# Kernel tuning notes

Hardware: AMD Instinct MI355X
Metric: run time of the kernel (lower is better)

The kernel has to match this reference:

```python
import jax, jax.numpy as jnp
import numpy as np

EMBED_DIM = 256
NUM_HEADS = 4
HEAD_DIM = EMBED_DIM // NUM_HEADS  # 64
FEAT_X = FEAT_Y = 64               # 64*64 = 4096 tokens
THETA = 10000.0


def _axial_cos_sin(dim, end_x, end_y, theta):
    # compute_axial_cis: dim//4 frequencies per spatial axis, concatenated -> [N, dim//2]
    f = 1.0 / (theta ** (np.arange(0, dim, 4)[: dim // 4].astype(np.float32) / dim))
    t = np.arange(end_x * end_y)
    tx = (t % end_x).astype(np.float32)
    ty = (t // end_x).astype(np.float32)
    ang = np.concatenate([np.outer(tx, f), np.outer(ty, f)], axis=-1)  # [N, dim//2]
    return jnp.asarray(np.cos(ang)), jnp.asarray(np.sin(ang))


def _apply_rope(x, cos, sin):
    # x: [B, H, N, D]; adjacent pairs (x[..., 2i], x[..., 2i+1]) are the complex parts
    xr = x.reshape(*x.shape[:-1], -1, 2)
    xa, xb = xr[..., 0], xr[..., 1]          # [B, H, N, D//2]
    oa = xa * cos - xb * sin                  # cos/sin: [N, D//2], broadcast
    ob = xa * sin + xb * cos
    return jnp.stack([oa, ob], axis=-1).reshape(x.shape)


def setup_inputs() -> dict:
    key = jax.random.key(0)
    ks = jax.random.split(key, 8)
    B, N, D = 1, FEAT_X * FEAT_Y, EMBED_DIM
    s = 0.02  # weight init scale
    return {
        "q": jax.random.normal(ks[0], (B, N, D), jnp.float32),
        "k": jax.random.normal(ks[1], (B, N, D), jnp.float32),
        "v": jax.random.normal(ks[2], (B, N, D), jnp.float32),
        "wq": jax.random.normal(ks[3], (D, D), jnp.float32) * s,
        "bq": jnp.zeros((D,), jnp.float32),
        "wk": jax.random.normal(ks[4], (D, D), jnp.float32) * s,
        "bk": jnp.zeros((D,), jnp.float32),
        "wv": jax.random.normal(ks[5], (D, D), jnp.float32) * s,
        "bv": jnp.zeros((D,), jnp.float32),
        "wo": jax.random.normal(ks[6], (D, D), jnp.float32) * s,
        "bo": jnp.zeros((D,), jnp.float32),
        "return_attn": 0,
        "num_k_exclude_rope": 0,
    }


def reference(q, k, v, wq, bq, wk, bk, wv, bv, wo, bo, return_attn, num_k_exclude_rope):
    B, Nq, D = q.shape
    H, hd = NUM_HEADS, HEAD_DIM
    # QKV projections (weights stored [in, out], equiv to torch Linear W.T)
    qp = (q @ wq + bq).reshape(B, Nq, H, hd).transpose(0, 2, 1, 3)   # [B,H,Nq,hd]
    kp = (k @ wk + bk).reshape(B, -1, H, hd).transpose(0, 2, 1, 3)   # [B,H,Nk,hd]
    vp = (v @ wv + bv).reshape(B, -1, H, hd).transpose(0, 2, 1, 3)
    # rotary encoding on q and the first (Nk - num_k_exclude_rope) keys
    cos, sin = _axial_cos_sin(hd, FEAT_X, FEAT_Y, THETA)
    qp = _apply_rope(qp, cos, sin)
    nkr = kp.shape[2] - num_k_exclude_rope  # static Python int
    if num_k_exclude_rope > 0:
        kp = jnp.concatenate([_apply_rope(kp[:, :, :nkr], cos, sin), kp[:, :, nkr:]], axis=2)
    else:
        kp = _apply_rope(kp, cos, sin)
    # SDPA (eval: dropout_p = 0)
    scale = 1.0 / jnp.sqrt(jnp.asarray(hd, qp.dtype))
    scores = jnp.einsum("bhqd,bhkd->bhqk", qp, kp) * scale
    attn = jax.nn.softmax(scores, axis=-1)
    out = jnp.einsum("bhqk,bhkd->bhqd", attn, vp)
    out = out.transpose(0, 2, 1, 3).reshape(B, Nq, D)
    out = out @ wo + bo
    if return_attn:
        return out, scores  # attn_weight = q @ k^T * scale (pre-softmax, as in source)
    return out
```

## Files before the change

kernel.cpp:

```cpp
#include <hip/hip_runtime.h>
#include <hip/hip_bf16.h>
#include <math.h>

#define NTOK 4096
#define DEMB 256
#define NHEAD 4
#define HD 64

typedef short bf16x8 __attribute__((ext_vector_type(8)));
typedef short bf16x4 __attribute__((ext_vector_type(4)));
typedef float f32x4 __attribute__((ext_vector_type(4)));

__device__ __forceinline__ unsigned short f2b(float f) {
  union { float f; unsigned u; } v; v.f = f;
  return (unsigned short)((v.u + 0x7FFFu + ((v.u >> 16) & 1u)) >> 16);
}
__device__ __forceinline__ unsigned pack2(float lo, float hi) {
  return (unsigned)f2b(lo) | ((unsigned)f2b(hi) << 16);
}

__global__ void wtrans_kernel(const float* wq, const float* wk, const float* wv,
                              const float* wo, unsigned short* wt) {
  int idx = blockIdx.x * 256 + threadIdx.x;
  int m = idx >> 16, rest = idx & 0xFFFF;
  int o = rest >> 8, i = rest & 255;
  const float* w = (m == 0) ? wq : (m == 1) ? wk : (m == 2) ? wv : wo;
  wt[idx] = f2b(w[i * 256 + o]);
}

__global__ void cs_kernel(float2* cs) {
  int idx = blockIdx.x * 256 + threadIdx.x;
  int n = idx >> 5, p = idx & 31;
  int j = p & 15;
  float f = powf(10000.0f, -(float)j / 16.0f);
  float ang = ((p < 16) ? (float)(n & 63) : (float)(n >> 6)) * f;
  cs[idx] = make_float2(cosf(ang), sinf(ang));
}

__global__ __launch_bounds__(256) void qkvproj_kernel(
    const float* q, const float* k, const float* v, const unsigned short* wt,
    const float* bq, const float* bk, const float* bv, const float2* cs,
    unsigned short* qp, unsigned short* kp, unsigned short* vt) {
  int which = blockIdx.z;
  int wave = threadIdx.x >> 6, lane = threadIdx.x & 63;
  int col = lane & 15, g = lane >> 4;
  int mbase = blockIdx.x * 64 + wave * 16;
  int nbase = blockIdx.y * 64;
  const float* X = (which == 0) ? q : (which == 1) ? k : v;
  const unsigned short* W = wt + which * 65536;
  const float* bias = (which == 0) ? bq : (which == 1) ? bk : bv;

  f32x4 acc[4] = {};
  const float* ap0 = X + (mbase + col) * 256 + g * 8;
#pragma unroll
  for (int ks = 0; ks < 256; ks += 32) {
    float4 a0 = *(const float4*)(ap0 + ks);
    float4 a1 = *(const float4*)(ap0 + ks + 4);
    bf16x8 af;
    af[0] = (short)f2b(a0.x); af[1] = (short)f2b(a0.y);
    af[2] = (short)f2b(a0.z); af[3] = (short)f2b(a0.w);
    af[4] = (short)f2b(a1.x); af[5] = (short)f2b(a1.y);
    af[6] = (short)f2b(a1.z); af[7] = (short)f2b(a1.w);
#pragma unroll
    for (int nt = 0; nt < 4; ++nt) {
      bf16x8 bf_ = *(const bf16x8*)(W + (nbase + nt * 16 + col) * 256 + ks + g * 8);
      acc[nt] = __builtin_amdgcn_mfma_f32_16x16x32_bf16(af, bf_, acc[nt], 0, 0, 0);
    }
  }

  if (which == 2) {
    int kpos = ((mbase >> 5) << 5) + 8 * g + 4 * ((mbase >> 4) & 1);
#pragma unroll
    for (int nt = 0; nt < 4; ++nt) {
      int c = nbase + nt * 16 + col;
      float b = bias[c];
      bf16x4 pk;
#pragma unroll
      for (int r = 0; r < 4; ++r) pk[r] = (short)f2b(acc[nt][r] + b);
      *(bf16x4*)(vt + c * NTOK + kpos) = pk;
    }
  } else {
    const float QSC = 0.18033688f;
    unsigned short* dst = (which == 0) ? qp : kp;
#pragma unroll
    for (int nt = 0; nt < 4; ++nt) {
      int c = nbase + nt * 16 + col;
      float b = bias[c];
#pragma unroll
      for (int r = 0; r < 4; ++r) {
        int t = mbase + g * 4 + r;
        float val = acc[nt][r] + b;
        float2 csv = cs[t * 32 + ((c & 63) >> 1)];
        float pv = __shfl_xor(val, 1);
        float sn = (c & 1) ? csv.y : -csv.y;
        val = val * csv.x + pv * sn;
        if (which == 0) val *= QSC;
        dst[((c >> 6) * NTOK + t) * HD + (c & 63)] = f2b(val);
      }
    }
  }
}

__global__ __launch_bounds__(512, 2) void attn_kernel(
    const unsigned short* qp, const unsigned short* kp,
    const unsigned short* vt, unsigned short* att) {
  __shared__ alignas(16) unsigned char lds[131072];
  int id = blockIdx.x;
  int xcd = id & 7;
  int head = xcd >> 1;
  int qtile = ((id >> 3) << 1) | (xcd & 1);
  int qb = qtile * 64;
  int w = threadIdx.x >> 6, lane = threadIdx.x & 63;
  int kg = w & 3, qg = w >> 2;
  int col = lane & 15, g = lane >> 4;

  const unsigned kb0 = (unsigned)(kg * 2) * 8192u;
  const unsigned vb0 = 65536u + (unsigned)(kg * 2) * 8192u;
  const unsigned short* kgp = kp + (head * NTOK + kg * 1024) * HD;
  const unsigned short* vgp = vt + head * HD * NTOK + kg * 1024;

  int tid2 = qg * 64 + lane;
  bf16x8 skr[4], svr[4];

  auto stage_issue = [&](int t) {
    const unsigned short* kq = kgp + t * 64 * HD;
    const unsigned short* vq = vgp + t * 64;
#pragma unroll
    for (int i = 0; i < 4; ++i) {
      int c = tid2 + i * 128, tok = c >> 3, part = c & 7;
      skr[i] = *(const bf16x8*)(kq + tok * HD + part * 8);
      svr[i] = *(const bf16x8*)(vq + tok * NTOK + part * 8);
    }
  };
  auto stage_write = [&](int buf) {
    unsigned kb = kb0 + (unsigned)buf * 8192u, vb = vb0 + (unsigned)buf * 8192u;
#pragma unroll
    for (int i = 0; i < 4; ++i) {
      int c = tid2 + i * 128, tok = c >> 3, part = c & 7;
      unsigned off = (unsigned)(tok * 128) + (unsigned)((part * 16) ^ ((tok & 7) << 4));
      *(bf16x8*)(lds + kb + off) = skr[i];
      *(bf16x8*)(lds + vb + off) = svr[i];
    }
  };

  bf16x8 qf[2][2];
  {
    const unsigned short* qr = qp + (head * NTOK + qb + qg * 32) * HD;
#pragma unroll
    for (int qt = 0; qt < 2; ++qt)
#pragma unroll
      for (int h2 = 0; h2 < 2; ++h2)
        qf[qt][h2] = *(const bf16x8*)(qr + (qt * 16 + col) * HD + h2 * 32 + g * 8);
  }

  stage_issue(0);
  stage_write(0);
  stage_issue(1);
  __syncthreads();

  f32x4 acco[4][2] = {};
  float mrow[2] = {-1e30f, -1e30f}, lrow[2] = {0.f, 0.f};

  for (int t = 0; t < 16; ++t) {
    int cur = t & 1;
    if (t < 15) {
      stage_write(cur ^ 1);
      if (t < 14) stage_issue(t + 2);
    }
    unsigned kb = kb0 + (unsigned)cur * 8192u, vb = vb0 + (unsigned)cur * 8192u;

    f32x4 st[4][2] = {};
#pragma unroll
    for (int mt = 0; mt < 4; ++mt) {
      int tok = mt * 16 + col;
      unsigned ro = kb + (unsigned)(tok * 128) + (unsigned)((g * 16) ^ ((tok & 7) << 4));
      bf16x8 kf0 = *(const bf16x8*)(lds + ro);
      bf16x8 kf1 = *(const bf16x8*)(lds + (ro ^ 64u));
#pragma unroll
      for (int qt = 0; qt < 2; ++qt) {
        st[mt][qt] = __builtin_amdgcn_mfma_f32_16x16x32_bf16(kf0, qf[qt][0], st[mt][qt], 0, 0, 0);
        st[mt][qt] = __builtin_amdgcn_mfma_f32_16x16x32_bf16(kf1, qf[qt][1], st[mt][qt], 0, 0, 0);
      }
    }

    float fac[2];
    unsigned pw[2][2][4];
#pragma unroll
    for (int qt = 0; qt < 2; ++qt) {
      float pm = mrow[qt];
#pragma unroll
      for (int mt = 0; mt < 4; ++mt)
#pragma unroll
        for (int r = 0; r < 4; ++r) pm = fmaxf(pm, st[mt][qt][r]);
      pm = fmaxf(pm, __shfl_xor(pm, 16));
      pm = fmaxf(pm, __shfl_xor(pm, 32));
      fac[qt] = exp2f(mrow[qt] - pm);
      mrow[qt] = pm;
      float ps = 0.f;
      float p[4][4];
#pragma unroll
      for (int mt = 0; mt < 4; ++mt)
#pragma unroll
        for (int r = 0; r < 4; ++r) {
          p[mt][r] = exp2f(st[mt][qt][r] - pm);
          ps += p[mt][r];
        }
      ps += __shfl_xor(ps, 16);
      ps += __shfl_xor(ps, 32);
      lrow[qt] = lrow[qt] * fac[qt] + ps;
#pragma unroll
      for (int kk = 0; kk < 2; ++kk) {
        pw[qt][kk][0] = pack2(p[2 * kk][0], p[2 * kk][1]);
        pw[qt][kk][1] = pack2(p[2 * kk][2], p[2 * kk][3]);
        pw[qt][kk][2] = pack2(p[2 * kk + 1][0], p[2 * kk + 1][1]);
        pw[qt][kk][3] = pack2(p[2 * kk + 1][2], p[2 * kk + 1][3]);
      }
    }

    float frow[2][4];
#pragma unroll
    for (int qt = 0; qt < 2; ++qt)
#pragma unroll
      for (int r = 0; r < 4; ++r) frow[qt][r] = __shfl(fac[qt], g * 4 + r);
#pragma unroll
    for (int nt = 0; nt < 4; ++nt)
#pragma unroll
      for (int qt = 0; qt < 2; ++qt) {
        acco[nt][qt][0] *= frow[qt][0]; acco[nt][qt][1] *= frow[qt][1];
        acco[nt][qt][2] *= frow[qt][2]; acco[nt][qt][3] *= frow[qt][3];
      }

#pragma unroll
    for (int kk = 0; kk < 2; ++kk) {
#pragma unroll
      for (int nt = 0; nt < 4; ++nt) {
        int d = nt * 16 + col;
        unsigned off = vb + (unsigned)(d * 128) +
                       (unsigned)((kk * 64 + g * 16) ^ ((d & 7) << 4));
        bf16x8 vf = *(const bf16x8*)(lds + off);
#pragma unroll
        for (int qt = 0; qt < 2; ++qt) {
          union { unsigned u[4]; bf16x8 v; } pf;
          pf.u[0] = pw[qt][kk][0]; pf.u[1] = pw[qt][kk][1];
          pf.u[2] = pw[qt][kk][2]; pf.u[3] = pw[qt][kk][3];
          acco[nt][qt] = __builtin_amdgcn_mfma_f32_16x16x32_bf16(pf.v, vf, acco[nt][qt], 0, 0, 0);
        }
      }
    }
    __syncthreads();
  }

  float* Om = (float*)lds;
  float* Ml = (float*)(lds + 65536);
#pragma unroll
  for (int nt = 0; nt < 4; ++nt)
#pragma unroll
    for (int qt = 0; qt < 2; ++qt)
#pragma unroll
      for (int r = 0; r < 4; ++r)
        Om[w * 2048 + (qt * 16 + g * 4 + r) * 64 + nt * 16 + col] = acco[nt][qt][r];
  if (g == 0) {
#pragma unroll
    for (int qt = 0; qt < 2; ++qt) {
      Ml[(w * 32 + qt * 16 + col) * 2 + 0] = mrow[qt];
      Ml[(w * 32 + qt * 16 + col) * 2 + 1] = lrow[qt];
    }
  }
  __syncthreads();

  int qg2 = threadIdx.x >> 8, qq = (threadIdx.x >> 3) & 31, d0 = (threadIdx.x & 7) * 8;
  float mx = -1e30f;
#pragma unroll
  for (int k2 = 0; k2 < 4; ++k2)
    mx = fmaxf(mx, Ml[((qg2 * 4 + k2) * 32 + qq) * 2]);
  float den = 0.f, num[8] = {};
#pragma unroll
  for (int k2 = 0; k2 < 4; ++k2) {
    int wv = qg2 * 4 + k2;
    float wgt = exp2f(Ml[(wv * 32 + qq) * 2] - mx);
    den += wgt * Ml[(wv * 32 + qq) * 2 + 1];
#pragma unroll
    for (int i = 0; i < 8; ++i) num[i] += wgt * Om[wv * 2048 + qq * 64 + d0 + i];
  }
  float inv = 1.0f / den;
  union { unsigned short s[8]; bf16x8 v; } ov;
#pragma unroll
  for (int i = 0; i < 8; ++i) ov.s[i] = f2b(num[i] * inv);
  *(bf16x8*)(att + (qb + qg2 * 32 + qq) * DEMB + head * HD + d0) = ov.v;
}

__global__ __launch_bounds__(256) void outproj_kernel(
    const unsigned short* att, const unsigned short* wt_o, const float* bo,
    float* out) {
  int wave = threadIdx.x >> 6, lane = threadIdx.x & 63;
  int col = lane & 15, g = lane >> 4;
  int mbase = blockIdx.x * 64 + wave * 16;
  int nbase = blockIdx.y * 64;
  f32x4 acc[4] = {};
#pragma unroll
  for (int ks = 0; ks < 256; ks += 32) {
    bf16x8 af = *(const bf16x8*)(att + (mbase + col) * 256 + ks + g * 8);
#pragma unroll
    for (int nt = 0; nt < 4; ++nt) {
      bf16x8 bf_ = *(const bf16x8*)(wt_o + (nbase + nt * 16 + col) * 256 + ks + g * 8);
      acc[nt] = __builtin_amdgcn_mfma_f32_16x16x32_bf16(af, bf_, acc[nt], 0, 0, 0);
    }
  }
#pragma unroll
  for (int nt = 0; nt < 4; ++nt) {
    int c = nbase + nt * 16 + col;
    float b = bo[c];
#pragma unroll
    for (int r = 0; r < 4; ++r)
      out[(mbase + g * 4 + r) * 256 + c] = acc[nt][r] + b;
  }
}

extern "C" void kernel_launch(void* const* d_in, const int* in_sizes, int n_in,
                              void* d_out, int out_size, void* d_ws, size_t ws_size,
                              hipStream_t stream) {
  const float* q  = (const float*)d_in[0];
  const float* k  = (const float*)d_in[1];
  const float* v  = (const float*)d_in[2];
  const float* wq = (const float*)d_in[3];
  const float* bq = (const float*)d_in[4];
  const float* wk = (const float*)d_in[5];
  const float* bk = (const float*)d_in[6];
  const float* wv = (const float*)d_in[7];
  const float* bv = (const float*)d_in[8];
  const float* wo = (const float*)d_in[9];
  const float* bo = (const float*)d_in[10];
  float* out = (float*)d_out;

  char* ws = (char*)d_ws;
  float2* cs        = (float2*)ws;
  unsigned short* wt = (unsigned short*)(ws + (1u << 20));
  unsigned short* qp = (unsigned short*)(ws + (1u << 20) + (512u << 10));
  unsigned short* kp = qp + NHEAD * NTOK * HD;
  unsigned short* vt = kp + NHEAD * NTOK * HD;
  unsigned short* att = vt + NHEAD * NTOK * HD;

  wtrans_kernel<<<1024, 256, 0, stream>>>(wq, wk, wv, wo, wt);
  cs_kernel<<<512, 256, 0, stream>>>(cs);
  qkvproj_kernel<<<dim3(64, 4, 3), 256, 0, stream>>>(q, k, v, wt, bq, bk, bv, cs,
                                                     qp, kp, vt);
  attn_kernel<<<256, 512, 0, stream>>>(qp, kp, vt, att);
  outproj_kernel<<<dim3(64, 4), 256, 0, stream>>>(att, wt + 3 * 65536, bo, out);
}
```

Before: 82.69 us.

## Split attention over key chunks across blocks and merge partials in a separate kernel

Each attention block now covers 256 queries (32 per wave across 8 waves) for one quarter of the keys, instead of 64 queries with the keys split across waves inside the block. LDS use drops from 128KB to 32KB. Each wave writes its unnormalized output plus its row max and sum to global workspace, and a new merge kernel combines the four key splits with a log-sum-exp rescale. The goal is more query reuse of each staged K/V tile and better occupancy. The cost is an extra kernel launch and a round trip of fp32 partials (about 16MB) through global memory.

Measured after the change: 87.22 us. 1.05x slower.

```diff
diff --git a/kernel.cpp b/kernel.cpp
--- a/kernel.cpp
+++ b/kernel.cpp
@@ -103,49 +103,40 @@
 
 __global__ __launch_bounds__(512, 2) void attn_kernel(
     const unsigned short* qp, const unsigned short* kp,
-    const unsigned short* vt, unsigned short* att) {
-  __shared__ alignas(16) unsigned char lds[131072];
+    const unsigned short* vt, float* pO, float* pml) {
+  __shared__ alignas(16) unsigned char lds[32768];
   int id = blockIdx.x;
   int xcd = id & 7;
   int head = xcd >> 1;
-  int qtile = ((id >> 3) << 1) | (xcd & 1);
-  int qb = qtile * 64;
+  int kshi = xcd & 1;
+  int rest = id >> 3;
+  int qtile = rest >> 1;
+  int ks = kshi * 2 + (rest & 1);
+  int qb = qtile * 256;
+  int slot = (head * 16 + qtile) * 4 + ks;
   int w = threadIdx.x >> 6, lane = threadIdx.x & 63;
-  int kg = w & 3, qg = w >> 2;
   int col = lane & 15, g = lane >> 4;
-
-  const unsigned kb0 = (unsigned)(kg * 2) * 8192u;
-  const unsigned vb0 = 65536u + (unsigned)(kg * 2) * 8192u;
-  const unsigned short* kgp = kp + (head * NTOK + kg * 1024) * HD;
-  const unsigned short* vgp = vt + head * HD * NTOK + kg * 1024;
-
-  int tid2 = qg * 64 + lane;
-  bf16x8 skr[4], svr[4];
-
+  int sid = threadIdx.x;
+  int stok = sid >> 3, spart = sid & 7;
+  unsigned soff = (unsigned)(stok * 128) +
+                  (unsigned)((spart * 16) ^ ((stok & 7) << 4));
+
+  const unsigned short* kgp = kp + (head * NTOK + ks * 1024) * HD;
+  const unsigned short* vgp = vt + head * HD * NTOK + ks * 1024;
+
+  bf16x8 skr, svr;
   auto stage_issue = [&](int t) {
-    const unsigned short* kq = kgp + t * 64 * HD;
-    const unsigned short* vq = vgp + t * 64;
-#pragma unroll
-    for (int i = 0; i < 4; ++i) {
-      int c = tid2 + i * 128, tok = c >> 3, part = c & 7;
-      skr[i] = *(const bf16x8*)(kq + tok * HD + part * 8);
-      svr[i] = *(const bf16x8*)(vq + tok * NTOK + part * 8);
-    }
+    skr = *(const bf16x8*)(kgp + (t * 64 + stok) * HD + spart * 8);
+    svr = *(const bf16x8*)(vgp + stok * NTOK + t * 64 + spart * 8);
   };
   auto stage_write = [&](int buf) {
-    unsigned kb = kb0 + (unsigned)buf * 8192u, vb = vb0 + (unsigned)buf * 8192u;
-#pragma unroll
-    for (int i = 0; i < 4; ++i) {
-      int c = tid2 + i * 128, tok = c >> 3, part = c & 7;
-      unsigned off = (unsigned)(tok * 128) + (unsigned)((part * 16) ^ ((tok & 7) << 4));
-      *(bf16x8*)(lds + kb + off) = skr[i];
-      *(bf16x8*)(lds + vb + off) = svr[i];
-    }
+    *(bf16x8*)(lds + (unsigned)buf * 16384u + soff) = skr;
+    *(bf16x8*)(lds + (unsigned)buf * 16384u + 8192u + soff) = svr;
   };
 
   bf16x8 qf[2][2];
   {
-    const unsigned short* qr = qp + (head * NTOK + qb + qg * 32) * HD;
+    const unsigned short* qr = qp + (head * NTOK + qb + w * 32) * HD;
 #pragma unroll
     for (int qt = 0; qt < 2; ++qt)
 #pragma unroll
@@ -167,7 +158,7 @@
       stage_write(cur ^ 1);
       if (t < 14) stage_issue(t + 2);
     }
-    unsigned kb = kb0 + (unsigned)cur * 8192u, vb = vb0 + (unsigned)cur * 8192u;
+    unsigned kb = (unsigned)cur * 16384u, vb = (unsigned)cur * 16384u + 8192u;
 
     f32x4 st[4][2] = {};
 #pragma unroll
@@ -250,43 +241,51 @@
     __syncthreads();
   }
 
-  float* Om = (float*)lds;
-  float* Ml = (float*)(lds + 65536);
 #pragma unroll
   for (int nt = 0; nt < 4; ++nt)
 #pragma unroll
     for (int qt = 0; qt < 2; ++qt)
 #pragma unroll
       for (int r = 0; r < 4; ++r)
-        Om[w * 2048 + (qt * 16 + g * 4 + r) * 64 + nt * 16 + col] = acco[nt][qt][r];
+        pO[slot * 16384 + (w * 32 + qt * 16 + g * 4 + r) * 64 + nt * 16 + col] =
+            acco[nt][qt][r];
   if (g == 0) {
 #pragma unroll
     for (int qt = 0; qt < 2; ++qt) {
-      Ml[(w * 32 + qt * 16 + col) * 2 + 0] = mrow[qt];
-      Ml[(w * 32 + qt * 16 + col) * 2 + 1] = lrow[qt];
-    }
-  }
-  __syncthreads();
-
-  int qg2 = threadIdx.x >> 8, qq = (threadIdx.x >> 3) & 31, d0 = (threadIdx.x & 7) * 8;
+      pml[slot * 512 + (w * 32 + qt * 16 + col) * 2 + 0] = mrow[qt];
+      pml[slot * 512 + (w * 32 + qt * 16 + col) * 2 + 1] = lrow[qt];
+    }
+  }
+}
+
+__global__ __launch_bounds__(256) void merge_kernel(
+    const float* pO, const float* pml, unsigned short* att) {
+  int bid = blockIdx.x;
+  int group = bid >> 2, quarter = bid & 3;
+  int head = group >> 4, qtile = group & 15;
+  int t = threadIdx.x;
+  int qloc = quarter * 64 + (t >> 2);
+  int d0 = (t & 3) * 16;
+  const float* mlb = pml + (group * 4) * 512 + qloc * 2;
   float mx = -1e30f;
 #pragma unroll
-  for (int k2 = 0; k2 < 4; ++k2)
-    mx = fmaxf(mx, Ml[((qg2 * 4 + k2) * 32 + qq) * 2]);
-  float den = 0.f, num[8] = {};
-#pragma unroll
-  for (int k2 = 0; k2 < 4; ++k2) {
-    int wv = qg2 * 4 + k2;
-    float wgt = exp2f(Ml[(wv * 32 + qq) * 2] - mx);
-    den += wgt * Ml[(wv * 32 + qq) * 2 + 1];
-#pragma unroll
-    for (int i = 0; i < 8; ++i) num[i] += wgt * Om[wv * 2048 + qq * 64 + d0 + i];
+  for (int ks = 0; ks < 4; ++ks) mx = fmaxf(mx, mlb[ks * 512]);
+  float den = 0.f, num[16] = {};
+#pragma unroll
+  for (int ks = 0; ks < 4; ++ks) {
+    float wgt = exp2f(mlb[ks * 512] - mx);
+    den += wgt * mlb[ks * 512 + 1];
+    const float* ob = pO + ((group * 4 + ks) * 256 + qloc) * 64 + d0;
+#pragma unroll
+    for (int i = 0; i < 16; ++i) num[i] += wgt * ob[i];
   }
   float inv = 1.0f / den;
-  union { unsigned short s[8]; bf16x8 v; } ov;
-#pragma unroll
-  for (int i = 0; i < 8; ++i) ov.s[i] = f2b(num[i] * inv);
-  *(bf16x8*)(att + (qb + qg2 * 32 + qq) * DEMB + head * HD + d0) = ov.v;
+  union { unsigned short s[16]; bf16x8 v[2]; } ov;
+#pragma unroll
+  for (int i = 0; i < 16; ++i) ov.s[i] = f2b(num[i] * inv);
+  unsigned short* dst = att + (qtile * 256 + qloc) * DEMB + head * HD + d0;
+  *(bf16x8*)dst = ov.v[0];
+  *(bf16x8*)(dst + 8) = ov.v[1];
 }
 
 __global__ __launch_bounds__(256) void outproj_kernel(
@@ -333,17 +332,20 @@
   float* out = (float*)d_out;
 
   char* ws = (char*)d_ws;
-  float2* cs        = (float2*)ws;
+  float2* cs         = (float2*)ws;
   unsigned short* wt = (unsigned short*)(ws + (1u << 20));
-  unsigned short* qp = (unsigned short*)(ws + (1u << 20) + (512u << 10));
+  unsigned short* qp = (unsigned short*)(ws + 1536u * 1024u);
   unsigned short* kp = qp + NHEAD * NTOK * HD;
   unsigned short* vt = kp + NHEAD * NTOK * HD;
   unsigned short* att = vt + NHEAD * NTOK * HD;
+  float* pO  = (float*)(ws + 9728u * 1024u);
+  float* pml = (float*)(ws + 26112u * 1024u);
 
   wtrans_kernel<<<1024, 256, 0, stream>>>(wq, wk, wv, wo, wt);
   cs_kernel<<<512, 256, 0, stream>>>(cs);
   qkvproj_kernel<<<dim3(64, 4, 3), 256, 0, stream>>>(q, k, v, wt, bq, bk, bv, cs,
                                                      qp, kp, vt);
-  attn_kernel<<<256, 512, 0, stream>>>(qp, kp, vt, att);
+  attn_kernel<<<256, 512, 0, stream>>>(qp, kp, vt, pO, pml);
+  merge_kernel<<<256, 256, 0, stream>>>(pO, pml, att);
   outproj_kernel<<<dim3(64, 4), 256, 0, stream>>>(att, wt + 3 * 65536, bo, out);
 }
```
